# Optimization experiments

Measured on AMD Instinct MI355X. Metric: run time of the kernel, lower is better.

Reference implementation:

```python
import jax, jax.numpy as jnp
from jax import lax
import numpy as np

B, T, NL = 512, 64, 32          # batch, timepoints per patient, n_labs
LAT, HID = 64, 128              # latent_dim, hidden_dim
SCALE, STEP, QPAD, TMAX = 365.0, 0.05, 2000, 2000


def setup_inputs() -> dict:
    key = jax.random.key(0)
    k = jax.random.split(key, 24)
    def rn(ki, shape, s=0.05):
        return jax.random.normal(ki, shape, jnp.float32) * s
    Din = 2 * NL + 1  # GRU input: labs, mask, dt
    return {
        "obs_vals": rn(k[0], (B, T, NL), 1.0),
        "age": jax.random.uniform(k[1], (B,), jnp.float32),
        "eps": rn(k[2], (B, LAT), 1.0),  # reparameterization noise (randn_like)
        "gru_Wih": rn(k[3], (Din, 3 * HID)), "gru_Whh": rn(k[4], (HID, 3 * HID)),
        "gru_bih": jnp.zeros((3 * HID,)), "gru_bhh": jnp.zeros((3 * HID,)),
        "Wmu": rn(k[5], (HID, LAT)), "bmu": jnp.zeros((LAT,)),
        "Wlv": rn(k[6], (HID, LAT)), "blv": jnp.zeros((LAT,)),
        "W1": rn(k[7], (LAT, HID)), "b1": jnp.zeros((HID,)),
        "W2": rn(k[8], (HID, HID)), "b2": jnp.zeros((HID,)),
        "W3": rn(k[9], (HID, LAT)), "b3": jnp.zeros((LAT,)),
        "Wo1": rn(k[10], (LAT, HID)), "bo1": jnp.zeros((HID,)),
        "Wo2": rn(k[11], (HID, NL)), "bo2": jnp.zeros((NL,)),
        "Ws1": rn(k[12], (LAT + 1, HID)), "bs1": jnp.zeros((HID,)),
        "Ws2": rn(k[13], (HID, 2)), "bs2": jnp.zeros((2,)),
        "obs_mask": jax.random.bernoulli(k[14], 0.7, (B, T, NL)),
        "timepoints": jnp.sort(jax.random.randint(k[15], (B, T), 0, TMAX), axis=1).astype(jnp.int32),
        "seq_lens": jax.random.randint(k[16], (B,), 1, T + 1).astype(jnp.int32),
    }


def reference(obs_vals, age, eps, gru_Wih, gru_Whh, gru_bih, gru_bhh,
              Wmu, bmu, Wlv, blv, W1, b1, W2, b2, W3, b3,
              Wo1, bo1, Wo2, bo2, Ws1, bs1, Ws2, bs2,
              obs_mask, timepoints, seq_lens):
    Bv, Tv, Dv = obs_vals.shape
    Hdim = gru_Whh.shape[0]
    tp = timepoints.astype(jnp.float32)

    # ---- RecognitionRNN (GRU over reversed sequence) ----
    dt = jnp.concatenate([jnp.zeros((Bv, 1)), tp[:, 1:] - tp[:, :-1]], axis=1)[..., None]
    maskf = obs_mask.astype(obs_vals.dtype)
    inp = jnp.concatenate([obs_vals * maskf, maskf, dt], axis=-1)  # [B,T,2*NL+1]
    x_seq = jnp.flip(inp, axis=1).transpose(1, 0, 2)  # [T,B,Din]

    def gru_step(h, x):
        gi = x @ gru_Wih + gru_bih
        gh = h @ gru_Whh + gru_bhh
        ir, iz, i_n = jnp.split(gi, 3, axis=-1)
        hr, hz, hn = jnp.split(gh, 3, axis=-1)
        r = jax.nn.sigmoid(ir + hr)
        zg = jax.nn.sigmoid(iz + hz)
        n = jnp.tanh(i_n + r * hn)
        h = (1.0 - zg) * n + zg * h
        return h, None

    h, _ = lax.scan(gru_step, jnp.zeros((Bv, Hdim), obs_vals.dtype), x_seq)
    mu = h @ Wmu + bmu
    logvar = h @ Wlv + blv
    z0 = mu + eps * jnp.exp(0.5 * logvar)  # reparameterize

    # ---- query times (padded unique; timepoints are >= 0 by construction) ----
    qd = jnp.unique(timepoints.reshape(-1), size=QPAD, fill_value=timepoints.max())
    query_t = qd.astype(jnp.float32) / SCALE  # [Q], nondecreasing

    # ---- torchdiffeq fixed-grid rk4 with step_size ----
    qnp = np.asarray(query_t)
    t0, t1 = float(qnp[0]), float(qnp[-1])
    niters = int(np.ceil((t1 - t0) / STEP + 1))
    grid = np.arange(niters) * STEP + t0
    if grid[-1] > t1:
        grid[-1] = t1
    grid = jnp.asarray(grid, jnp.float32)  # [G]

    def ode_f(z):
        return jnp.tanh(jnp.tanh(z @ W1 + b1) @ W2 + b2) @ W3 + b3

    def rk4_step(y, hstep):
        k1 = ode_f(y)
        k2 = ode_f(y + 0.5 * hstep * k1)
        k3 = ode_f(y + 0.5 * hstep * k2)
        k4 = ode_f(y + hstep * k3)
        y2 = y + (hstep / 6.0) * (k1 + 2.0 * k2 + 2.0 * k3 + k4)
        return y2, y2

    _, ys = lax.scan(rk4_step, z0, grid[1:] - grid[:-1])
    ys = jnp.concatenate([z0[None], ys], axis=0)  # [G,B,L]

    # linear interpolation of grid states at query_t (torchdiffeq behavior)
    gi = jnp.clip(jnp.searchsorted(grid, query_t, side="right") - 1, 0, grid.shape[0] - 2)
    tl, tr = grid[gi], grid[gi + 1]
    w = ((query_t - tl) / jnp.where(tr - tl == 0, 1.0, tr - tl))[:, None, None]
    z_traj = ys[gi] * (1.0 - w) + ys[gi + 1] * w  # [Q,B,L]

    # ---- reconstruction loss (vectorized over B,T) ----
    tq = tp / SCALE  # [B,T]
    idx_q = jnp.argmin(jnp.abs(query_t[None, None, :] - tq[:, :, None]), axis=-1)  # [B,T]
    z_bt = z_traj[idx_q, jnp.arange(Bv)[:, None]]  # [B,T,L]
    x_hat = jax.nn.relu(z_bt @ Wo1 + bo1) @ Wo2 + bo2  # [B,T,NL]
    valid = (jnp.arange(Tv)[None, :] < seq_lens[:, None]).astype(obs_vals.dtype)[..., None]
    m = maskf * valid
    n_obs = m.sum()
    recon = jnp.where(n_obs > 0,
                      (m * (x_hat - obs_vals) ** 2).sum() / jnp.maximum(n_obs, 1.0),
                      0.0)

    kl = -0.5 * jnp.mean(jnp.sum(1.0 + logvar - mu ** 2 - jnp.exp(logvar), axis=-1))

    # ---- z_eval at last observed timepoint per patient ----
    last_tp = jnp.take_along_axis(tp, (seq_lens - 1)[:, None], axis=1)[:, 0] / SCALE  # [B]
    idx_e = jnp.argmin(jnp.abs(query_t[None, :] - last_tp[:, None]), axis=-1)  # [B]
    z_eval = z_traj[idx_e, jnp.arange(Bv)]  # [B,L]
    log_hazard = jax.nn.relu(jnp.concatenate([z_eval, age[:, None]], axis=-1) @ Ws1 + bs1) @ Ws2 + bs2
    return log_hazard, recon, kl, z_eval
```

## Files before the change

kernel.cpp:

```cpp
#include <hip/hip_runtime.h>
#include <hip/hip_bf16.h>
#include <math.h>

#define B 512
#define T 64
#define NL 32
#define LAT 64
#define HID 128
#define DIN 65
#define G3 384
#define FSCALE 365.0f
#define MAXGRID 128
#define R_ODE 16

#define WS_MIN   0
#define WS_MAX   1
#define WS_NIT   2
#define WS_KL    3
#define WS_RE    4
#define WS_NO    5
#define WS_GRID  8
#define WS_Z0    (WS_GRID + MAXGRID)
#define WS_YS    (WS_Z0 + B*LAT)

typedef __attribute__((ext_vector_type(8))) __bf16 bf16x8;
typedef __attribute__((ext_vector_type(4))) float f32x4;

static __device__ __forceinline__ float tanh_fast(float x){
    float t = __builtin_amdgcn_exp2f(x * 2.8853900817779268f);
    return 1.0f - 2.0f * __builtin_amdgcn_rcpf(t + 1.0f);
}
static __device__ __forceinline__ float sigmoid_fast(float x){
    return __builtin_amdgcn_rcpf(1.0f + __builtin_amdgcn_exp2f(-1.4426950408889634f * x));
}

__global__ void k_init(const int* __restrict__ tp, float* wsf){
    int* wsi = (int*)wsf;
    __shared__ int smin[256], smax[256];
    int tid = threadIdx.x;
    int mn = 2147483647, mx = -2147483647-1;
    for (int i = tid; i < B*T; i += 256){ int v = tp[i]; mn = min(mn,v); mx = max(mx,v); }
    smin[tid]=mn; smax[tid]=mx; __syncthreads();
    for (int s=128; s>0; s>>=1){
        if (tid<s){ smin[tid]=min(smin[tid],smin[tid+s]); smax[tid]=max(smax[tid],smax[tid+s]); }
        __syncthreads();
    }
    if (tid==0){
        wsi[WS_MIN]=smin[0]; wsi[WS_MAX]=smax[0];
        wsf[WS_KL]=0.f; wsf[WS_RE]=0.f; wsf[WS_NO]=0.f;
    }
}

__global__ void k_grid(float* wsf){
    int* wsi=(int*)wsf;
    float t0f = (float)wsi[WS_MIN] / FSCALE;
    float t1f = (float)wsi[WS_MAX] / FSCALE;
    double t0d = (double)t0f, t1d = (double)t1f;
    int nit = (int)ceil((t1d-t0d)/0.05 + 1.0);
    if (nit < 1) nit = 1;
    if (nit > MAXGRID) nit = MAXGRID;
    if (threadIdx.x==0) wsi[WS_NIT] = nit;
    int k = threadIdx.x;
    if (k < nit){
        double g = (double)k * 0.05 + t0d;
        if (k == nit-1 && g > t1d) g = t1d;
        wsf[WS_GRID + k] = (float)g;
    }
}

__global__ __launch_bounds__(512) void k_gru(
    const float* __restrict__ obs, const float* __restrict__ eps,
    const float* __restrict__ Wih, const float* __restrict__ Whh,
    const float* __restrict__ bih, const float* __restrict__ bhh,
    const float* __restrict__ Wmu, const float* __restrict__ bmu,
    const float* __restrict__ Wlv, const float* __restrict__ blv,
    const int* __restrict__ maskI, const int* __restrict__ tp,
    float* wsf)
{
    const int b0 = blockIdx.x * 16;
    const int tid = threadIdx.x;
    const int w = tid >> 6, lane = tid & 63;
    const int g = lane >> 4, c = lane & 15;
    const int xr = tid >> 5, xl = tid & 31;

    __shared__ __align__(16) __bf16 xh[16][232];
    __shared__ int   tps[16][64];
    __shared__ float dts[16];
    __shared__ float lvs[16][64];
    __shared__ float red[8];

    ((int2*)tps)[tid] = ((const int2*)(tp + (size_t)b0*T))[tid];
    {
        unsigned* xz = (unsigned*)&xh[0][0];
        #pragma unroll
        for (int i=0;i<1856;i+=512) xz[i+tid] = 0u;
    }

    bf16x8 wr[6], wz[6], wi[2], wh[4];
    #pragma unroll
    for (int q=0;q<6;++q){
        int kt = q<2 ? q : q+1;
        #pragma unroll
        for (int e=0;e<8;++e){
            int k = kt*32 + g*8 + e;
            float vr, vz;
            if (k < 64){ vr = Wih[k*G3 + 16*w+c];      vz = Wih[k*G3 + 128+16*w+c]; }
            else       { vr = Whh[(k-96)*G3 + 16*w+c]; vz = Whh[(k-96)*G3 + 128+16*w+c]; }
            wr[q][e] = (__bf16)vr; wz[q][e] = (__bf16)vz;
        }
    }
    #pragma unroll
    for (int q=0;q<2;++q)
        #pragma unroll
        for (int e=0;e<8;++e)
            wi[q][e] = (__bf16)Wih[(q*32+g*8+e)*G3 + 256+16*w+c];
    #pragma unroll
    for (int q=0;q<4;++q)
        #pragma unroll
        for (int e=0;e<8;++e)
            wh[q][e] = (__bf16)Whh[(q*32+g*8+e)*G3 + 256+16*w+c];
    const float wdr = Wih[64*G3 + 16*w+c];
    const float wdz = Wih[64*G3 + 128+16*w+c];
    const float wdn = Wih[64*G3 + 256+16*w+c];
    const float rb  = bih[16*w+c]     + bhh[16*w+c];
    const float zb  = bih[128+16*w+c] + bhh[128+16*w+c];
    const float inb = bih[256+16*w+c];
    const float hnb = bhh[256+16*w+c];

    __syncthreads();

    {
        float mv = (float)maskI[((size_t)(b0+xr)*T + 63)*NL + xl];
        float ov = obs[((size_t)(b0+xr)*T + 63)*NL + xl];
        xh[xr][xl]    = (__bf16)(ov*mv);
        xh[xr][32+xl] = (__bf16)mv;
        if (xl==0) dts[xr] = (float)(tps[xr][63]-tps[xr][62]);
    }

    float hold[4] = {0.f,0.f,0.f,0.f};

    for (int s=0;s<T;++s){
        const int t = T-1-s;
        __syncthreads();
        bf16x8 A0 = *(const bf16x8*)&xh[c][0*32 + g*8];
        bf16x8 A1 = *(const bf16x8*)&xh[c][1*32 + g*8];
        bf16x8 A2 = *(const bf16x8*)&xh[c][3*32 + g*8];
        bf16x8 A3 = *(const bf16x8*)&xh[c][4*32 + g*8];
        bf16x8 A4 = *(const bf16x8*)&xh[c][5*32 + g*8];
        bf16x8 A5 = *(const bf16x8*)&xh[c][6*32 + g*8];
        const float dt0=dts[4*g], dt1=dts[4*g+1], dt2=dts[4*g+2], dt3=dts[4*g+3];
        float ov=0.f, mvn=0.f; const int tn = t-1;
        if (s < T-1){
            mvn = (float)maskI[((size_t)(b0+xr)*T + tn)*NL + xl];
            ov  = obs[((size_t)(b0+xr)*T + tn)*NL + xl];
        }
        f32x4 racc={0,0,0,0}, zacc={0,0,0,0}, inacc={0,0,0,0}, hnacc={0,0,0,0};
        racc  = __builtin_amdgcn_mfma_f32_16x16x32_bf16(A0, wr[0], racc, 0,0,0);
        zacc  = __builtin_amdgcn_mfma_f32_16x16x32_bf16(A0, wz[0], zacc, 0,0,0);
        inacc = __builtin_amdgcn_mfma_f32_16x16x32_bf16(A0, wi[0], inacc,0,0,0);
        hnacc = __builtin_amdgcn_mfma_f32_16x16x32_bf16(A2, wh[0], hnacc,0,0,0);
        racc  = __builtin_amdgcn_mfma_f32_16x16x32_bf16(A1, wr[1], racc, 0,0,0);
        zacc  = __builtin_amdgcn_mfma_f32_16x16x32_bf16(A1, wz[1], zacc, 0,0,0);
        inacc = __builtin_amdgcn_mfma_f32_16x16x32_bf16(A1, wi[1], inacc,0,0,0);
        hnacc = __builtin_amdgcn_mfma_f32_16x16x32_bf16(A3, wh[1], hnacc,0,0,0);
        racc  = __builtin_amdgcn_mfma_f32_16x16x32_bf16(A2, wr[2], racc, 0,0,0);
        zacc  = __builtin_amdgcn_mfma_f32_16x16x32_bf16(A2, wz[2], zacc, 0,0,0);
        hnacc = __builtin_amdgcn_mfma_f32_16x16x32_bf16(A4, wh[2], hnacc,0,0,0);
        racc  = __builtin_amdgcn_mfma_f32_16x16x32_bf16(A3, wr[3], racc, 0,0,0);
        zacc  = __builtin_amdgcn_mfma_f32_16x16x32_bf16(A3, wz[3], zacc, 0,0,0);
        hnacc = __builtin_amdgcn_mfma_f32_16x16x32_bf16(A5, wh[3], hnacc,0,0,0);
        racc  = __builtin_amdgcn_mfma_f32_16x16x32_bf16(A4, wr[4], racc, 0,0,0);
        zacc  = __builtin_amdgcn_mfma_f32_16x16x32_bf16(A4, wz[4], zacc, 0,0,0);
        racc  = __builtin_amdgcn_mfma_f32_16x16x32_bf16(A5, wr[5], racc, 0,0,0);
        zacc  = __builtin_amdgcn_mfma_f32_16x16x32_bf16(A5, wz[5], zacc, 0,0,0);
        float hnew[4]; const float dtv[4] = {dt0,dt1,dt2,dt3};
        #pragma unroll
        for (int j=0;j<4;++j){
            float dv = dtv[j];
            float r  = sigmoid_fast(racc[j] + rb + dv*wdr);
            float zg = sigmoid_fast(zacc[j] + zb + dv*wdz);
            float n  = tanh_fast(inacc[j] + inb + dv*wdn + r*(hnacc[j] + hnb));
            float hv = (1.f - zg)*n + zg*hold[j];
            hold[j] = hv; hnew[j] = hv;
        }
        __syncthreads();
        #pragma unroll
        for (int j=0;j<4;++j) xh[4*g+j][96+16*w+c] = (__bf16)hnew[j];
        if (s < T-1){
            xh[xr][xl]    = (__bf16)(ov*mvn);
            xh[xr][32+xl] = (__bf16)mvn;
            if (xl==0) dts[xr] = (tn>0) ? (float)(tps[xr][tn]-tps[xr][tn-1]) : 0.f;
        }
    }
    __syncthreads();

    const int col4 = 16*(w&3)+c;
    bf16x8 Ah0 = *(const bf16x8*)&xh[c][96+0*32+g*8];
    bf16x8 Ah1 = *(const bf16x8*)&xh[c][96+1*32+g*8];
    bf16x8 Ah2 = *(const bf16x8*)&xh[c][96+2*32+g*8];
    bf16x8 Ah3 = *(const bf16x8*)&xh[c][96+3*32+g*8];
    const float* Wm = (w<4)? Wmu : Wlv;
    f32x4 acc={0,0,0,0};
    {
        bf16x8 bf0,bf1,bf2,bf3;
        #pragma unroll
        for (int e=0;e<8;++e){
            bf0[e] = (__bf16)Wm[(0*32+g*8+e)*LAT + col4];
            bf1[e] = (__bf16)Wm[(1*32+g*8+e)*LAT + col4];
            bf2[e] = (__bf16)Wm[(2*32+g*8+e)*LAT + col4];
            bf3[e] = (__bf16)Wm[(3*32+g*8+e)*LAT + col4];
        }
        acc = __builtin_amdgcn_mfma_f32_16x16x32_bf16(Ah0, bf0, acc, 0,0,0);
        acc = __builtin_amdgcn_mfma_f32_16x16x32_bf16(Ah1, bf1, acc, 0,0,0);
        acc = __builtin_amdgcn_mfma_f32_16x16x32_bf16(Ah2, bf2, acc, 0,0,0);
        acc = __builtin_amdgcn_mfma_f32_16x16x32_bf16(Ah3, bf3, acc, 0,0,0);
    }
    const float mbias = (w<4)? bmu[col4] : blv[col4];
    if (w>=4){
        #pragma unroll
        for (int j=0;j<4;++j) lvs[4*g+j][col4] = acc[j] + mbias;
    }
    __syncthreads();
    if (w<4){
        float kl = 0.f;
        #pragma unroll
        for (int j=0;j<4;++j){
            float mu = acc[j] + mbias;
            float lv = lvs[4*g+j][col4];
            int row = b0 + 4*g + j;
            float z0 = mu + eps[(size_t)row*LAT + col4]*expf(0.5f*lv);
            wsf[WS_Z0 + (size_t)row*LAT + col4] = z0;
            wsf[WS_YS + (size_t)row*LAT + col4] = z0;
            kl += 1.f + lv - mu*mu - expf(lv);
        }
        #pragma unroll
        for (int off=32; off>0; off>>=1) kl += __shfl_xor(kl, off);
        if (lane==0) red[w] = kl;
    }
    __syncthreads();
    if (tid==0) atomicAdd(&wsf[WS_KL], red[0]+red[1]+red[2]+red[3]);
}

__global__ __launch_bounds__(512) void k_ode(
    const float* __restrict__ W1, const float* __restrict__ b1,
    const float* __restrict__ W2, const float* __restrict__ b2,
    const float* __restrict__ W3, const float* __restrict__ b3,
    float* wsf)
{
    const int b0 = blockIdx.x * R_ODE;
    const int tid = threadIdx.x;
    const int w = tid >> 6, lane = tid & 63;
    const int g = lane >> 4, c = lane & 15;
    const int w3c = 16*(w&3) + c;
    const int* wsi = (const int*)wsf;
    const int nit = wsi[WS_NIT];

    __shared__ __align__(16) __bf16 zin[16][72];
    __shared__ __align__(16) __bf16 h1s[16][136];
    __shared__ __align__(16) __bf16 h2s[16][136];
    __shared__ float gls[MAXGRID];

    bf16x8 w1f[2], w2f[4], w3f[4];
    #pragma unroll
    for (int q=0;q<2;++q)
        #pragma unroll
        for (int e=0;e<8;++e)
            w1f[q][e] = (__bf16)W1[(q*32+g*8+e)*HID + 16*w+c];
    #pragma unroll
    for (int q=0;q<4;++q)
        #pragma unroll
        for (int e=0;e<8;++e)
            w2f[q][e] = (__bf16)W2[(q*32+g*8+e)*HID + 16*w+c];
    #pragma unroll
    for (int q=0;q<4;++q)
        #pragma unroll
        for (int e=0;e<8;++e)
            w3f[q][e] = (__bf16)W3[(q*32+g*8+e)*LAT + w3c];
    const float b1v = b1[16*w+c];
    const float b2v = b2[16*w+c];
    const float b3v = b3[w3c];

    float y[4], facc[4];
    if (w < 4){
        #pragma unroll
        for (int j=0;j<4;++j){
            y[j] = wsf[WS_Z0 + (size_t)(b0 + 4*g + j)*LAT + w3c];
            zin[4*g+j][w3c] = (__bf16)y[j];
            facc[j] = 0.f;
        }
    }
    for (int kk=tid; kk<MAXGRID; kk+=512) gls[kk] = wsf[WS_GRID+kk];
    __syncthreads();

    for (int i=0; i<nit-1; ++i){
        float h = gls[i+1]-gls[i];
        #pragma unroll
        for (int sub=0; sub<4; ++sub){
            f32x4 a1 = {0.f,0.f,0.f,0.f};
            {
                bf16x8 az0 = *(const bf16x8*)&zin[c][g*8];
                bf16x8 az1 = *(const bf16x8*)&zin[c][32+g*8];
                a1 = __builtin_amdgcn_mfma_f32_16x16x32_bf16(az0, w1f[0], a1, 0,0,0);
                a1 = __builtin_amdgcn_mfma_f32_16x16x32_bf16(az1, w1f[1], a1, 0,0,0);
            }
            #pragma unroll
            for (int j=0;j<4;++j)
                h1s[4*g+j][16*w+c] = (__bf16)tanh_fast(a1[j] + b1v);
            __syncthreads();
            f32x4 c2a = {0.f,0.f,0.f,0.f}, c2b = {0.f,0.f,0.f,0.f};
            {
                bf16x8 aq0 = *(const bf16x8*)&h1s[c][g*8];
                bf16x8 aq1 = *(const bf16x8*)&h1s[c][32+g*8];
                bf16x8 aq2 = *(const bf16x8*)&h1s[c][64+g*8];
                bf16x8 aq3 = *(const bf16x8*)&h1s[c][96+g*8];
                c2a = __builtin_amdgcn_mfma_f32_16x16x32_bf16(aq0, w2f[0], c2a, 0,0,0);
                c2b = __builtin_amdgcn_mfma_f32_16x16x32_bf16(aq2, w2f[2], c2b, 0,0,0);
                c2a = __builtin_amdgcn_mfma_f32_16x16x32_bf16(aq1, w2f[1], c2a, 0,0,0);
                c2b = __builtin_amdgcn_mfma_f32_16x16x32_bf16(aq3, w2f[3], c2b, 0,0,0);
            }
            #pragma unroll
            for (int j=0;j<4;++j)
                h2s[4*g+j][16*w+c] = (__bf16)tanh_fast((c2a[j]+c2b[j]) + b2v);
            __syncthreads();
            if (w < 4){
                f32x4 c3a = {0.f,0.f,0.f,0.f}, c3b = {0.f,0.f,0.f,0.f};
                bf16x8 aq0 = *(const bf16x8*)&h2s[c][g*8];
                bf16x8 aq1 = *(const bf16x8*)&h2s[c][32+g*8];
                bf16x8 aq2 = *(const bf16x8*)&h2s[c][64+g*8];
                bf16x8 aq3 = *(const bf16x8*)&h2s[c][96+g*8];
                c3a = __builtin_amdgcn_mfma_f32_16x16x32_bf16(aq0, w3f[0], c3a, 0,0,0);
                c3b = __builtin_amdgcn_mfma_f32_16x16x32_bf16(aq2, w3f[2], c3b, 0,0,0);
                c3a = __builtin_amdgcn_mfma_f32_16x16x32_bf16(aq1, w3f[1], c3a, 0,0,0);
                c3b = __builtin_amdgcn_mfma_f32_16x16x32_bf16(aq3, w3f[3], c3b, 0,0,0);
                #pragma unroll
                for (int j=0;j<4;++j){
                    float f = (c3a[j]+c3b[j]) + b3v;
                    float zn;
                    if (sub==0){ facc[j] = f;         zn = fmaf(0.5f*h, f, y[j]); }
                    else if (sub==1){ facc[j] += 2.f*f; zn = fmaf(0.5f*h, f, y[j]); }
                    else if (sub==2){ facc[j] += 2.f*f; zn = fmaf(h, f, y[j]); }
                    else {
                        facc[j] += f;
                        y[j] = fmaf(h*(1.0f/6.0f), facc[j], y[j]);
                        zn = y[j];
                        wsf[WS_YS + ((size_t)(i+1)*B + (b0+4*g+j))*LAT + w3c] = y[j];
                    }
                    zin[4*g+j][w3c] = (__bf16)zn;
                }
            }
            __syncthreads();
        }
    }
}

__global__ __launch_bounds__(512) void k_recon(
    const float* __restrict__ obs, const int* __restrict__ maskI,
    const int* __restrict__ tp, const int* __restrict__ seq,
    const float* __restrict__ Wo1, const float* __restrict__ bo1,
    const float* __restrict__ Wo2, const float* __restrict__ bo2,
    float* wsf)
{
    const int b = blockIdx.x, tid = threadIdx.x;
    const int w = tid >> 6, lane = tid & 63;
    const int g = lane >> 4, c = lane & 15;
    __shared__ __align__(16) __bf16 zbt[64][72];
    __shared__ __align__(16) __bf16 hb[64][136];
    __shared__ float gls[MAXGRID];
    __shared__ float red[16];
    const int* wsi=(const int*)wsf;
    const int nit = wsi[WS_NIT];
    for (int i=tid;i<MAXGRID;i+=512) gls[i]=wsf[WS_GRID+i];

    bf16x8 wo1f[2], wo2f[4];
    #pragma unroll
    for (int q=0;q<2;++q)
        #pragma unroll
        for (int e=0;e<8;++e)
            wo1f[q][e] = (__bf16)Wo1[(q*32+g*8+e)*HID + 16*w+c];
    {
        int n = w & 1;
        #pragma unroll
        for (int q=0;q<4;++q)
            #pragma unroll
            for (int e=0;e<8;++e)
                wo2f[q][e] = (__bf16)Wo2[(q*32+g*8+e)*NL + 16*n+c];
    }
    const float bo1v = bo1[16*w+c];
    const float bo2v = bo2[16*(w&1)+c];
    const int sl = seq[b];
    __syncthreads();

    {
        int t = tid >> 3, seg = tid & 7;
        float tq = (float)tp[b*T+t] / FSCALE;
        int lo=0, hi=nit;
        while (lo<hi){ int mid=(lo+hi)>>1; if (gls[mid]<=tq) lo=mid+1; else hi=mid; }
        int k = lo-1; if (k<0) k=0; if (nit>=2 && k>nit-2) k=nit-2; if (nit<2) k=0;
        float wq=0.f;
        if (nit>=2){ float tl=gls[k], tr=gls[k+1]; float den=(tr-tl==0.f)?1.f:(tr-tl); wq=(tq-tl)/den; }
        size_t o0 = (size_t)WS_YS + ((size_t)k*B + b)*LAT + seg*8;
        float4 za0 = *(const float4*)&wsf[o0];
        float4 za1 = *(const float4*)&wsf[o0+4];
        float4 zb0, zb1;
        if (nit>=2){
            zb0 = *(const float4*)&wsf[o0 + (size_t)B*LAT];
            zb1 = *(const float4*)&wsf[o0 + (size_t)B*LAT + 4];
        } else { zb0 = za0; zb1 = za1; }
        __bf16* dst = &zbt[t][seg*8];
        dst[0] = (__bf16)(za0.x*(1.f-wq)+zb0.x*wq);
        dst[1] = (__bf16)(za0.y*(1.f-wq)+zb0.y*wq);
        dst[2] = (__bf16)(za0.z*(1.f-wq)+zb0.z*wq);
        dst[3] = (__bf16)(za0.w*(1.f-wq)+zb0.w*wq);
        dst[4] = (__bf16)(za1.x*(1.f-wq)+zb1.x*wq);
        dst[5] = (__bf16)(za1.y*(1.f-wq)+zb1.y*wq);
        dst[6] = (__bf16)(za1.z*(1.f-wq)+zb1.z*wq);
        dst[7] = (__bf16)(za1.w*(1.f-wq)+zb1.w*wq);
    }
    __syncthreads();

    #pragma unroll
    for (int m=0;m<4;++m){
        f32x4 acc = {0.f,0.f,0.f,0.f};
        bf16x8 a0 = *(const bf16x8*)&zbt[16*m+c][g*8];
        bf16x8 a1 = *(const bf16x8*)&zbt[16*m+c][32+g*8];
        acc = __builtin_amdgcn_mfma_f32_16x16x32_bf16(a0, wo1f[0], acc, 0,0,0);
        acc = __builtin_amdgcn_mfma_f32_16x16x32_bf16(a1, wo1f[1], acc, 0,0,0);
        #pragma unroll
        for (int j=0;j<4;++j)
            hb[16*m+4*g+j][16*w+c] = (__bf16)fmaxf(acc[j] + bo1v, 0.f);
    }
    __syncthreads();

    float esum = 0.f, ncnt = 0.f;
    {
        int m = w >> 1, n = w & 1;
        f32x4 ca = {0.f,0.f,0.f,0.f}, cb = {0.f,0.f,0.f,0.f};
        bf16x8 a0 = *(const bf16x8*)&hb[16*m+c][g*8];
        bf16x8 a1 = *(const bf16x8*)&hb[16*m+c][32+g*8];
        bf16x8 a2 = *(const bf16x8*)&hb[16*m+c][64+g*8];
        bf16x8 a3 = *(const bf16x8*)&hb[16*m+c][96+g*8];
        ca = __builtin_amdgcn_mfma_f32_16x16x32_bf16(a0, wo2f[0], ca, 0,0,0);
        cb = __builtin_amdgcn_mfma_f32_16x16x32_bf16(a2, wo2f[2], cb, 0,0,0);
        ca = __builtin_amdgcn_mfma_f32_16x16x32_bf16(a1, wo2f[1], ca, 0,0,0);
        cb = __builtin_amdgcn_mfma_f32_16x16x32_bf16(a3, wo2f[3], cb, 0,0,0);
        #pragma unroll
        for (int j=0;j<4;++j){
            int t = 16*m + 4*g + j;
            int col = 16*n + c;
            float xh2 = (ca[j]+cb[j]) + bo2v;
            float mv = (float)maskI[(b*T+t)*NL+col] * ((t<sl)?1.f:0.f);
            float d = xh2 - obs[(b*T+t)*NL+col];
            esum = fmaf(mv*d, d, esum);
            ncnt += mv;
        }
    }
    #pragma unroll
    for (int off=32; off>0; off>>=1){
        esum += __shfl_xor(esum, off);
        ncnt += __shfl_xor(ncnt, off);
    }
    if (lane==0){ red[w] = esum; red[8+w] = ncnt; }
    __syncthreads();
    if (tid==0){
        float s=0.f, nn=0.f;
        #pragma unroll
        for (int i=0;i<8;++i){ s += red[i]; nn += red[8+i]; }
        atomicAdd(&wsf[WS_RE], s);
        atomicAdd(&wsf[WS_NO], nn);
    }
}

__global__ __launch_bounds__(128) void k_surv(
    const float* __restrict__ age, const int* __restrict__ tp, const int* __restrict__ seq,
    const float* __restrict__ Ws1, const float* __restrict__ bs1,
    const float* __restrict__ Ws2, const float* __restrict__ bs2,
    float* wsf, float* out)
{
    int b=blockIdx.x, tid=threadIdx.x;
    __shared__ float gls[MAXGRID];
    __shared__ float ze[64];
    __shared__ float pred[4];
    const int* wsi=(const int*)wsf; int nit=wsi[WS_NIT];
    for (int i=tid;i<MAXGRID;i+=128) gls[i]=wsf[WS_GRID+i];
    __syncthreads();
    int sl = seq[b];
    float tq = (float)tp[b*T + sl-1] / FSCALE;
    int lo=0,hi=nit;
    while(lo<hi){int mid=(lo+hi)>>1; if (gls[mid]<=tq) lo=mid+1; else hi=mid;}
    int k=lo-1; if(k<0)k=0; if(nit>=2 && k>nit-2)k=nit-2; if (nit<2) k=0;
    float w=0.f;
    if (nit>=2){ float tl=gls[k],tr=gls[k+1]; float den=(tr-tl==0.f)?1.f:(tr-tl); w=(tq-tl)/den; }
    if (tid<LAT){
        size_t o0 = (size_t)WS_YS + ((size_t)k*B+b)*LAT+tid;
        float zl = wsf[o0]*(1.f-w) + ((nit>=2)? wsf[o0+(size_t)B*LAT]*w : 0.f);
        ze[tid]=zl;
        out[1026 + b*LAT + tid] = zl;
    }
    __syncthreads();
    float hj = bs1[tid];
    #pragma unroll 8
    for (int l=0;l<LAT;++l) hj = fmaf(ze[l], Ws1[l*HID+tid], hj);
    hj = fmaf(age[b], Ws1[LAT*HID+tid], hj);
    hj = fmaxf(hj,0.f);
    float p0 = hj*Ws2[tid*2+0], p1 = hj*Ws2[tid*2+1];
    #pragma unroll
    for (int off=32;off>0;off>>=1){ p0 += __shfl_down(p0,off); p1 += __shfl_down(p1,off); }
    int wv = tid>>6;
    if ((tid&63)==0){ pred[wv*2]=p0; pred[wv*2+1]=p1; }
    __syncthreads();
    if (tid==0){
        out[b*2+0] = bs2[0] + pred[0]+pred[2];
        out[b*2+1] = bs2[1] + pred[1]+pred[3];
    }
}

__global__ void k_fin(float* wsf, float* out){
    float n = wsf[WS_NO];
    out[1024] = (n>0.f) ? (wsf[WS_RE]/fmaxf(n,1.f)) : 0.f;
    out[1025] = -0.5f * (wsf[WS_KL] / (float)B);
}

extern "C" void kernel_launch(void* const* d_in, const int* in_sizes, int n_in,
                              void* d_out, int out_size, void* d_ws, size_t ws_size,
                              hipStream_t stream) {
    const float* obs   = (const float*)d_in[0];
    const float* age   = (const float*)d_in[1];
    const float* eps   = (const float*)d_in[2];
    const float* Wih   = (const float*)d_in[3];
    const float* Whh   = (const float*)d_in[4];
    const float* bih   = (const float*)d_in[5];
    const float* bhh   = (const float*)d_in[6];
    const float* Wmu   = (const float*)d_in[7];
    const float* bmu   = (const float*)d_in[8];
    const float* Wlv   = (const float*)d_in[9];
    const float* blv   = (const float*)d_in[10];
    const float* W1    = (const float*)d_in[11];
    const float* b1    = (const float*)d_in[12];
    const float* W2    = (const float*)d_in[13];
    const float* b2    = (const float*)d_in[14];
    const float* W3    = (const float*)d_in[15];
    const float* b3    = (const float*)d_in[16];
    const float* Wo1   = (const float*)d_in[17];
    const float* bo1   = (const float*)d_in[18];
    const float* Wo2   = (const float*)d_in[19];
    const float* bo2   = (const float*)d_in[20];
    const float* Ws1   = (const float*)d_in[21];
    const float* bs1   = (const float*)d_in[22];
    const float* Ws2   = (const float*)d_in[23];
    const float* bs2   = (const float*)d_in[24];
    const int*   maskI = (const int*)d_in[25];
    const int*   tp    = (const int*)d_in[26];
    const int*   seq   = (const int*)d_in[27];
    float* wsf = (float*)d_ws;
    float* out = (float*)d_out;

    k_init<<<1, 256, 0, stream>>>(tp, wsf);
    k_grid<<<1, 128, 0, stream>>>(wsf);
    k_gru<<<B/16, 512, 0, stream>>>(obs, eps, Wih, Whh, bih, bhh, Wmu, bmu, Wlv, blv,
                                    maskI, tp, wsf);
    k_ode<<<B/R_ODE, 512, 0, stream>>>(W1, b1, W2, b2, W3, b3, wsf);
    k_recon<<<B, 512, 0, stream>>>(obs, maskI, tp, seq, Wo1, bo1, Wo2, bo2, wsf);
    k_surv<<<B, 128, 0, stream>>>(age, tp, seq, Ws1, bs1, Ws2, bs2, wsf, out);
    k_fin<<<1, 1, 0, stream>>>(wsf, out);
}
```

Measured before the change: 541.8 us.

## Process 64 batch rows per ODE block with 2D warp tiling

The ODE kernel now handles 64 batch rows per block instead of 16, with each of 8 warps owning a 16-row tile and half of the output columns. Each warp issues several MFMAs per layer from the same A fragment, and all warps take part in the third layer instead of only four. This cuts the grid from 32 to 8 blocks, so far fewer CUs run the serial RK4 loop, but each block does four times the work between barriers. It also needs more registers for weight fragments, which may raise register pressure.

```diff
diff --git a/kernel.cpp b/kernel.cpp
--- a/kernel.cpp
+++ b/kernel.cpp
@@ -11,7 +11,6 @@
 #define G3 384
 #define FSCALE 365.0f
 #define MAXGRID 128
-#define R_ODE 16
 
 #define WS_MIN   0
 #define WS_MAX   1
@@ -247,48 +246,61 @@
     const float* __restrict__ W3, const float* __restrict__ b3,
     float* wsf)
 {
-    const int b0 = blockIdx.x * R_ODE;
+    const int b0 = blockIdx.x * 64;
     const int tid = threadIdx.x;
     const int w = tid >> 6, lane = tid & 63;
     const int g = lane >> 4, c = lane & 15;
-    const int w3c = 16*(w&3) + c;
+    const int mt = w >> 1, ch = w & 1;
+    const int r0 = 16*mt;
     const int* wsi = (const int*)wsf;
     const int nit = wsi[WS_NIT];
 
-    __shared__ __align__(16) __bf16 zin[16][72];
-    __shared__ __align__(16) __bf16 h1s[16][136];
-    __shared__ __align__(16) __bf16 h2s[16][136];
+    __shared__ __align__(16) __bf16 zin[64][72];
+    __shared__ __align__(16) __bf16 h1s[64][136];
+    __shared__ __align__(16) __bf16 h2s[64][136];
     __shared__ float gls[MAXGRID];
 
-    bf16x8 w1f[2], w2f[4], w3f[4];
-    #pragma unroll
-    for (int q=0;q<2;++q)
-        #pragma unroll
-        for (int e=0;e<8;++e)
-            w1f[q][e] = (__bf16)W1[(q*32+g*8+e)*HID + 16*w+c];
-    #pragma unroll
-    for (int q=0;q<4;++q)
-        #pragma unroll
-        for (int e=0;e<8;++e)
-            w2f[q][e] = (__bf16)W2[(q*32+g*8+e)*HID + 16*w+c];
-    #pragma unroll
-    for (int q=0;q<4;++q)
-        #pragma unroll
-        for (int e=0;e<8;++e)
-            w3f[q][e] = (__bf16)W3[(q*32+g*8+e)*LAT + w3c];
-    const float b1v = b1[16*w+c];
-    const float b2v = b2[16*w+c];
-    const float b3v = b3[w3c];
-
-    float y[4], facc[4];
-    if (w < 4){
+    bf16x8 w1f[4][2];
+    bf16x8 w2f[4][4];
+    bf16x8 w3f[2][4];
+    #pragma unroll
+    for (int t=0;t<4;++t)
+        #pragma unroll
+        for (int q=0;q<2;++q)
+            #pragma unroll
+            for (int e=0;e<8;++e)
+                w1f[t][q][e] = (__bf16)W1[(q*32+g*8+e)*HID + 64*ch+16*t+c];
+    #pragma unroll
+    for (int t=0;t<4;++t)
+        #pragma unroll
+        for (int q=0;q<4;++q)
+            #pragma unroll
+            for (int e=0;e<8;++e)
+                w2f[t][q][e] = (__bf16)W2[(q*32+g*8+e)*HID + 64*ch+16*t+c];
+    #pragma unroll
+    for (int t=0;t<2;++t)
+        #pragma unroll
+        for (int q=0;q<4;++q)
+            #pragma unroll
+            for (int e=0;e<8;++e)
+                w3f[t][q][e] = (__bf16)W3[(q*32+g*8+e)*LAT + 32*ch+16*t+c];
+    float b1v[4], b2v[4], b3v[2];
+    #pragma unroll
+    for (int t=0;t<4;++t){ b1v[t] = b1[64*ch+16*t+c]; b2v[t] = b2[64*ch+16*t+c]; }
+    #pragma unroll
+    for (int t=0;t<2;++t) b3v[t] = b3[32*ch+16*t+c];
+
+    float y[2][4], facc[2][4];
+    #pragma unroll
+    for (int t=0;t<2;++t)
         #pragma unroll
         for (int j=0;j<4;++j){
-            y[j] = wsf[WS_Z0 + (size_t)(b0 + 4*g + j)*LAT + w3c];
-            zin[4*g+j][w3c] = (__bf16)y[j];
-            facc[j] = 0.f;
-        }
-    }
+            int row = b0 + r0 + 4*g + j;
+            int col = 32*ch + 16*t + c;
+            y[t][j] = wsf[WS_Z0 + (size_t)row*LAT + col];
+            zin[r0+4*g+j][col] = (__bf16)y[t][j];
+            facc[t][j] = 0.f;
+        }
     for (int kk=tid; kk<MAXGRID; kk+=512) gls[kk] = wsf[WS_GRID+kk];
     __syncthreads();
 
@@ -296,56 +308,65 @@
         float h = gls[i+1]-gls[i];
         #pragma unroll
         for (int sub=0; sub<4; ++sub){
-            f32x4 a1 = {0.f,0.f,0.f,0.f};
             {
-                bf16x8 az0 = *(const bf16x8*)&zin[c][g*8];
-                bf16x8 az1 = *(const bf16x8*)&zin[c][32+g*8];
-                a1 = __builtin_amdgcn_mfma_f32_16x16x32_bf16(az0, w1f[0], a1, 0,0,0);
-                a1 = __builtin_amdgcn_mfma_f32_16x16x32_bf16(az1, w1f[1], a1, 0,0,0);
+                bf16x8 az0 = *(const bf16x8*)&zin[r0+c][g*8];
+                bf16x8 az1 = *(const bf16x8*)&zin[r0+c][32+g*8];
+                #pragma unroll
+                for (int t=0;t<4;++t){
+                    f32x4 acc = {0.f,0.f,0.f,0.f};
+                    acc = __builtin_amdgcn_mfma_f32_16x16x32_bf16(az0, w1f[t][0], acc, 0,0,0);
+                    acc = __builtin_amdgcn_mfma_f32_16x16x32_bf16(az1, w1f[t][1], acc, 0,0,0);
+                    #pragma unroll
+                    for (int j=0;j<4;++j)
+                        h1s[r0+4*g+j][64*ch+16*t+c] = (__bf16)tanh_fast(acc[j] + b1v[t]);
+                }
             }
-            #pragma unroll
-            for (int j=0;j<4;++j)
-                h1s[4*g+j][16*w+c] = (__bf16)tanh_fast(a1[j] + b1v);
             __syncthreads();
-            f32x4 c2a = {0.f,0.f,0.f,0.f}, c2b = {0.f,0.f,0.f,0.f};
             {
-                bf16x8 aq0 = *(const bf16x8*)&h1s[c][g*8];
-                bf16x8 aq1 = *(const bf16x8*)&h1s[c][32+g*8];
-                bf16x8 aq2 = *(const bf16x8*)&h1s[c][64+g*8];
-                bf16x8 aq3 = *(const bf16x8*)&h1s[c][96+g*8];
-                c2a = __builtin_amdgcn_mfma_f32_16x16x32_bf16(aq0, w2f[0], c2a, 0,0,0);
-                c2b = __builtin_amdgcn_mfma_f32_16x16x32_bf16(aq2, w2f[2], c2b, 0,0,0);
-                c2a = __builtin_amdgcn_mfma_f32_16x16x32_bf16(aq1, w2f[1], c2a, 0,0,0);
-                c2b = __builtin_amdgcn_mfma_f32_16x16x32_bf16(aq3, w2f[3], c2b, 0,0,0);
+                bf16x8 aq0 = *(const bf16x8*)&h1s[r0+c][g*8];
+                bf16x8 aq1 = *(const bf16x8*)&h1s[r0+c][32+g*8];
+                bf16x8 aq2 = *(const bf16x8*)&h1s[r0+c][64+g*8];
+                bf16x8 aq3 = *(const bf16x8*)&h1s[r0+c][96+g*8];
+                #pragma unroll
+                for (int t=0;t<4;++t){
+                    f32x4 ca = {0.f,0.f,0.f,0.f}, cb = {0.f,0.f,0.f,0.f};
+                    ca = __builtin_amdgcn_mfma_f32_16x16x32_bf16(aq0, w2f[t][0], ca, 0,0,0);
+                    cb = __builtin_amdgcn_mfma_f32_16x16x32_bf16(aq2, w2f[t][2], cb, 0,0,0);
+                    ca = __builtin_amdgcn_mfma_f32_16x16x32_bf16(aq1, w2f[t][1], ca, 0,0,0);
+                    cb = __builtin_amdgcn_mfma_f32_16x16x32_bf16(aq3, w2f[t][3], cb, 0,0,0);
+                    #pragma unroll
+                    for (int j=0;j<4;++j)
+                        h2s[r0+4*g+j][64*ch+16*t+c] = (__bf16)tanh_fast((ca[j]+cb[j]) + b2v[t]);
+                }
             }
-            #pragma unroll
-            for (int j=0;j<4;++j)
-                h2s[4*g+j][16*w+c] = (__bf16)tanh_fast((c2a[j]+c2b[j]) + b2v);
             __syncthreads();
-            if (w < 4){
-                f32x4 c3a = {0.f,0.f,0.f,0.f}, c3b = {0.f,0.f,0.f,0.f};
-                bf16x8 aq0 = *(const bf16x8*)&h2s[c][g*8];
-                bf16x8 aq1 = *(const bf16x8*)&h2s[c][32+g*8];
-                bf16x8 aq2 = *(const bf16x8*)&h2s[c][64+g*8];
-                bf16x8 aq3 = *(const bf16x8*)&h2s[c][96+g*8];
-                c3a = __builtin_amdgcn_mfma_f32_16x16x32_bf16(aq0, w3f[0], c3a, 0,0,0);
-                c3b = __builtin_amdgcn_mfma_f32_16x16x32_bf16(aq2, w3f[2], c3b, 0,0,0);
-                c3a = __builtin_amdgcn_mfma_f32_16x16x32_bf16(aq1, w3f[1], c3a, 0,0,0);
-                c3b = __builtin_amdgcn_mfma_f32_16x16x32_bf16(aq3, w3f[3], c3b, 0,0,0);
+            {
+                bf16x8 aq0 = *(const bf16x8*)&h2s[r0+c][g*8];
+                bf16x8 aq1 = *(const bf16x8*)&h2s[r0+c][32+g*8];
+                bf16x8 aq2 = *(const bf16x8*)&h2s[r0+c][64+g*8];
+                bf16x8 aq3 = *(const bf16x8*)&h2s[r0+c][96+g*8];
                 #pragma unroll
-                for (int j=0;j<4;++j){
-                    float f = (c3a[j]+c3b[j]) + b3v;
-                    float zn;
-                    if (sub==0){ facc[j] = f;         zn = fmaf(0.5f*h, f, y[j]); }
-                    else if (sub==1){ facc[j] += 2.f*f; zn = fmaf(0.5f*h, f, y[j]); }
-                    else if (sub==2){ facc[j] += 2.f*f; zn = fmaf(h, f, y[j]); }
-                    else {
-                        facc[j] += f;
-                        y[j] = fmaf(h*(1.0f/6.0f), facc[j], y[j]);
-                        zn = y[j];
-                        wsf[WS_YS + ((size_t)(i+1)*B + (b0+4*g+j))*LAT + w3c] = y[j];
+                for (int t=0;t<2;++t){
+                    f32x4 ca = {0.f,0.f,0.f,0.f}, cb = {0.f,0.f,0.f,0.f};
+                    ca = __builtin_amdgcn_mfma_f32_16x16x32_bf16(aq0, w3f[t][0], ca, 0,0,0);
+                    cb = __builtin_amdgcn_mfma_f32_16x16x32_bf16(aq2, w3f[t][2], cb, 0,0,0);
+                    ca = __builtin_amdgcn_mfma_f32_16x16x32_bf16(aq1, w3f[t][1], ca, 0,0,0);
+                    cb = __builtin_amdgcn_mfma_f32_16x16x32_bf16(aq3, w3f[t][3], cb, 0,0,0);
+                    #pragma unroll
+                    for (int j=0;j<4;++j){
+                        float f = (ca[j]+cb[j]) + b3v[t];
+                        float zn;
+                        if (sub==0){ facc[t][j] = f;         zn = fmaf(0.5f*h, f, y[t][j]); }
+                        else if (sub==1){ facc[t][j] += 2.f*f; zn = fmaf(0.5f*h, f, y[t][j]); }
+                        else if (sub==2){ facc[t][j] += 2.f*f; zn = fmaf(h, f, y[t][j]); }
+                        else {
+                            facc[t][j] += f;
+                            y[t][j] = fmaf(h*(1.0f/6.0f), facc[t][j], y[t][j]);
+                            zn = y[t][j];
+                            wsf[WS_YS + ((size_t)(i+1)*B + (b0+r0+4*g+j))*LAT + 32*ch+16*t+c] = y[t][j];
+                        }
+                        zin[r0+4*g+j][32*ch+16*t+c] = (__bf16)zn;
                     }
-                    zin[4*g+j][w3c] = (__bf16)zn;
                 }
             }
             __syncthreads();
@@ -558,7 +579,7 @@
     k_grid<<<1, 128, 0, stream>>>(wsf);
     k_gru<<<B/16, 512, 0, stream>>>(obs, eps, Wih, Whh, bih, bhh, Wmu, bmu, Wlv, blv,
                                     maskI, tp, wsf);
-    k_ode<<<B/R_ODE, 512, 0, stream>>>(W1, b1, W2, b2, W3, b3, wsf);
+    k_ode<<<B/64, 512, 0, stream>>>(W1, b1, W2, b2, W3, b3, wsf);
     k_recon<<<B, 512, 0, stream>>>(obs, maskI, tp, seq, Wo1, bo1, Wo2, bo2, wsf);
     k_surv<<<B, 128, 0, stream>>>(age, tp, seq, Ws1, bs1, Ws2, bs2, wsf, out);
     k_fin<<<1, 1, 0, stream>>>(wsf, out);
```

Measured after the change: 1.096 ms. 2.02x slower.
